# Optimization experiments

Hardware: AMD Instinct MI355X
Metric: run time of the kernel (lower is better)

Reference implementation:

```python
import jax, jax.numpy as jnp
import numpy as np

B, N, DIM, HEADS, RED = 8, 1024, 768, 12, 2
CR = DIM // RED  # 384 reduced channel dim
HD = CR // HEADS  # 32 head dim
EPS = 1e-5


def layer_norm(x, g, b):
    mu = jnp.mean(x, axis=-1, keepdims=True)
    var = jnp.var(x, axis=-1, keepdims=True)
    return (x - mu) * jax.lax.rsqrt(var + EPS) * g + b


def setup_inputs() -> dict:
    key = jax.random.key(0)
    ks = jax.random.split(key, 8)
    s_in = 1.0 / np.sqrt(DIM)
    s_cr = 1.0 / np.sqrt(CR)
    return {
        "x": jax.random.normal(ks[0], (B, N, DIM), dtype=jnp.float32),
        "ln0_g": jnp.ones((DIM,), jnp.float32),
        "ln0_b": jnp.zeros((DIM,), jnp.float32),
        "w_proj": jax.random.normal(ks[1], (CR, DIM), jnp.float32) * s_in,  # conv1x1 -> linear
        "b_proj": jnp.zeros((CR,), jnp.float32),
        "ln1_g": jnp.ones((CR,), jnp.float32),
        "ln1_b": jnp.zeros((CR,), jnp.float32),
        "wq": jax.random.normal(ks[2], (CR, CR), jnp.float32) * s_cr,
        "wk": jax.random.normal(ks[3], (CR, CR), jnp.float32) * s_cr,
        "wv": jax.random.normal(ks[4], (CR, CR), jnp.float32) * s_cr,
    }


def attention(y, wq, wk, wv):
    # y: [B, N, CR]; 1x1 conv == linear on channel dim
    def heads(w):
        return (y @ w.T).reshape(B, N, HEADS, HD).transpose(0, 2, 1, 3)  # [B,H,N,D]
    q, k, v = heads(wq), heads(wk), heads(wv)
    scale = HD ** -0.5
    attn = jax.nn.softmax(jnp.einsum("bhnd,bhmd->bhnm", q, k) * scale, axis=-1)
    out = jnp.einsum("bhnm,bhmd->bhnd", attn, v)  # [B,H,N,D]
    return out.transpose(0, 2, 1, 3).reshape(B, N, CR)


def reference(x, ln0_g, ln0_b, w_proj, b_proj, ln1_g, ln1_b, wq, wk, wv):
    h = layer_norm(x, ln0_g, ln0_b) @ w_proj.T + b_proj  # [B,N,CR]
    y = layer_norm(h, ln1_g, ln1_b)
    return h + attention(y, wq, wk, wv)
```

## Files before the change

### kernel.cpp

```cpp
#include <hip/hip_runtime.h>
#include <math.h>

#define BB 8
#define NN 1024
#define DIM 768
#define HEADS 12
#define CR 384
#define HD 32
#define MROWS (BB*NN)
#define EPS 1e-5f
#define SCALE_Q 0.25503486f

typedef __attribute__((ext_vector_type(8))) __bf16 bf16x8;
typedef __attribute__((ext_vector_type(8))) unsigned short u16x8;
typedef __attribute__((ext_vector_type(4))) float f32x4;

__device__ __forceinline__ unsigned short f2bf(float f) {
    unsigned int u = __float_as_uint(f);
    u += 0x7fffu + ((u >> 16) & 1u);
    return (unsigned short)(u >> 16);
}

__device__ __forceinline__ unsigned int packbf2(float lo, float hi) {
    return (unsigned int)f2bf(lo) | ((unsigned int)f2bf(hi) << 16);
}

__device__ __forceinline__ void async_cp16(const unsigned short* g, unsigned short* l) {
    __builtin_amdgcn_global_load_lds(
        (const __attribute__((address_space(1))) unsigned int*)g,
        (__attribute__((address_space(3))) unsigned int*)l, 16, 0, 0);
}

__global__ __launch_bounds__(256) void ln_bf16(
    const float* __restrict__ A, int K,
    const float* __restrict__ g, const float* __restrict__ bt,
    unsigned short* __restrict__ Y)
{
    const int row = blockIdx.x;
    const int t = threadIdx.x;
    const int nv = K >> 2;
    const float* a = A + (size_t)row * K;
    float4 val = make_float4(0.f, 0.f, 0.f, 0.f);
    float s = 0.f, ss = 0.f;
    if (t < nv) {
        val = ((const float4*)a)[t];
        s = val.x + val.y + val.z + val.w;
        ss = val.x * val.x + val.y * val.y + val.z * val.z + val.w * val.w;
    }
    for (int off = 32; off; off >>= 1) {
        s  += __shfl_down(s, off, 64);
        ss += __shfl_down(ss, off, 64);
    }
    __shared__ float rS[4], rSS[4];
    __shared__ float sh_mu, sh_rs;
    int lane = t & 63, w = t >> 6;
    if (lane == 0) { rS[w] = s; rSS[w] = ss; }
    __syncthreads();
    if (t == 0) {
        float S = rS[0] + rS[1] + rS[2] + rS[3];
        float SS = rSS[0] + rSS[1] + rSS[2] + rSS[3];
        float m = S / K;
        sh_mu = m;
        sh_rs = rsqrtf(SS / K - m * m + EPS);
    }
    __syncthreads();
    if (t < nv) {
        float m = sh_mu, r = sh_rs;
        float4 gv = ((const float4*)g)[t];
        float4 bv = ((const float4*)bt)[t];
        ushort4 o = make_ushort4(
            f2bf((val.x - m) * r * gv.x + bv.x),
            f2bf((val.y - m) * r * gv.y + bv.y),
            f2bf((val.z - m) * r * gv.z + bv.z),
            f2bf((val.w - m) * r * gv.w + bv.w));
        ((ushort4*)(Y + (size_t)row * K))[t] = o;
    }
}

__global__ __launch_bounds__(256) void cast_weights(
    const float* __restrict__ wp, const float* __restrict__ wq,
    const float* __restrict__ wk, const float* __restrict__ wv,
    unsigned short* __restrict__ wpo, unsigned short* __restrict__ wqkvo)
{
    int i = blockIdx.x * 256 + threadIdx.x;
    const float* src; unsigned short* dst; int off;
    if (i < 73728) { src = wp; dst = wpo; off = i; }
    else {
        int j = i - 73728;
        int sel = j / 36864; off = j % 36864;
        src = sel == 0 ? wq : (sel == 1 ? wk : wv);
        dst = wqkvo + (size_t)sel * 147456;
    }
    float4 v = ((const float4*)src)[off];
    ushort4 o = make_ushort4(f2bf(v.x), f2bf(v.y), f2bf(v.z), f2bf(v.w));
    ((ushort4*)dst)[off] = o;
}

template<int KD, int MODE>
__global__ __launch_bounds__(256) void gemm_mfma(
    const unsigned short* __restrict__ A,
    const unsigned short* __restrict__ W,
    const float* __restrict__ bias,
    void* __restrict__ C0, void* __restrict__ C1)
{
    __shared__ unsigned short Asm[2 * 128 * 32];
    __shared__ unsigned short Bsm[2 * 128 * 32];
    const int t = threadIdx.x;
    const int wave = t >> 6, lane = t & 63;
    const int l15 = lane & 15, quad = lane >> 4;
    const int m0 = blockIdx.y * 128;
    const int n0 = blockIdx.x * 128;
    const int wm = (wave & 1) * 64, wn = (wave >> 1) * 64;

    const int srow = lane >> 2;
    const int skq  = (lane & 3) * 8;
    const unsigned short* gA = A + (size_t)(m0 + wave * 32 + srow) * KD + skq;
    const unsigned short* gB = W + (size_t)(n0 + wave * 32 + srow) * KD + skq;
    unsigned short* lA = Asm + wave * 1024;
    unsigned short* lB = Bsm + wave * 1024;

    constexpr int NIT = KD / 32;
    async_cp16(gA, lA);
    async_cp16(gA + (size_t)16 * KD, lA + 512);
    async_cp16(gB, lB);
    async_cp16(gB + (size_t)16 * KD, lB + 512);

    f32x4 acc[4][4];
#pragma unroll
    for (int i = 0; i < 4; i++)
#pragma unroll
        for (int j = 0; j < 4; j++) acc[i][j] = (f32x4){0.f, 0.f, 0.f, 0.f};

    for (int it = 0; it < NIT; it++) {
        __syncthreads();
        const int cur = it & 1;
        if (it + 1 < NIT) {
            const int noff = (cur ^ 1) * 4096;
            async_cp16(gA + (it + 1) * 32, lA + noff);
            async_cp16(gA + (size_t)16 * KD + (it + 1) * 32, lA + noff + 512);
            async_cp16(gB + (it + 1) * 32, lB + noff);
            async_cp16(gB + (size_t)16 * KD + (it + 1) * 32, lB + noff + 512);
        }
        const unsigned short* Ab = Asm + cur * 4096;
        const unsigned short* Bb = Bsm + cur * 4096;
        bf16x8 af[4], bfr[4];
#pragma unroll
        for (int i = 0; i < 4; i++)
            af[i] = *(const bf16x8*)(Ab + (wm + i * 16 + l15) * 32 + quad * 8);
#pragma unroll
        for (int j = 0; j < 4; j++)
            bfr[j] = *(const bf16x8*)(Bb + (wn + j * 16 + l15) * 32 + quad * 8);
#pragma unroll
        for (int i = 0; i < 4; i++)
#pragma unroll
            for (int j = 0; j < 4; j++)
                acc[i][j] = __builtin_amdgcn_mfma_f32_16x16x32_bf16(af[i], bfr[j], acc[i][j], 0, 0, 0);
    }

    if constexpr (MODE == 0) {
        float* C = (float*)C0;
        float bv[4];
#pragma unroll
        for (int j = 0; j < 4; j++) bv[j] = bias[n0 + wn + j * 16 + l15];
#pragma unroll
        for (int i = 0; i < 4; i++)
#pragma unroll
            for (int j = 0; j < 4; j++)
#pragma unroll
                for (int reg = 0; reg < 4; reg++) {
                    int row = m0 + wm + i * 16 + quad * 4 + reg;
                    int col = n0 + wn + j * 16 + l15;
                    C[(size_t)row * CR + col] = acc[i][j][reg] + bv[j];
                }
    } else {
        unsigned short* Cqk = (unsigned short*)C0;
        unsigned short* Vt  = (unsigned short*)C1;
#pragma unroll
        for (int i = 0; i < 4; i++)
#pragma unroll
            for (int j = 0; j < 4; j++) {
                const int colbase = n0 + wn + j * 16;
                const int token0 = m0 + wm + i * 16 + quad * 4;
                if (colbase < DIM) {
                    const float sc = (colbase < CR) ? SCALE_Q : 1.f;
#pragma unroll
                    for (int reg = 0; reg < 4; reg++)
                        Cqk[(size_t)(token0 + reg) * DIM + colbase + l15] = f2bf(acc[i][j][reg] * sc);
                } else {
                    const int ch = colbase - DIM + l15;
                    uint2 pk;
                    pk.x = packbf2(acc[i][j][0], acc[i][j][1]);
                    pk.y = packbf2(acc[i][j][2], acc[i][j][3]);
                    *(uint2*)(Vt + (size_t)ch * MROWS + token0) = pk;
                }
            }
    }
}

__global__ __launch_bounds__(256) void attn_mfma(
    const unsigned short* __restrict__ qk,
    const unsigned short* __restrict__ vt,
    const float* __restrict__ h, float* __restrict__ out)
{
    const int qt = blockIdx.x;
    const int bh = blockIdx.y;
    const int b = bh / HEADS, head = bh % HEADS;
    const int hc = head * HD;
    const int t = threadIdx.x;
    const int wave = t >> 6, lane = t & 63;
    const int l15 = lane & 15, quad = lane >> 4;
    const int q0 = qt * 64;

    __shared__ unsigned short Ks[64 * 40];
    __shared__ unsigned short Vs[32 * 72];
    __shared__ unsigned short Ps[4][16 * 72];
    unsigned short* Pw = Ps[wave];

    bf16x8 qa = *(const bf16x8*)(qk + (size_t)(b * NN + q0 + wave * 16 + l15) * DIM + hc + quad * 8);

    const int rr = t >> 2, seg = t & 3;
    const unsigned short* gK = qk + (size_t)(b * NN + rr) * DIM + CR + hc + seg * 8;
    const int vch = wave * 8 + (lane >> 3), vko = (lane & 7) * 8;
    const unsigned short* gV = vt + (size_t)(hc + vch) * MROWS + b * NN + vko;

    u16x8 kreg = *(const u16x8*)gK;
    u16x8 vreg = *(const u16x8*)gV;

    f32x4 o[2] = {{0.f,0.f,0.f,0.f},{0.f,0.f,0.f,0.f}};
    float lpart = 0.f;

    for (int kt = 0; kt < 16; kt++) {
        __syncthreads();
        *(u16x8*)(Ks + rr * 40 + seg * 8) = kreg;
        *(u16x8*)(Vs + vch * 72 + vko) = vreg;
        if (kt < 15) {
            kreg = *(const u16x8*)(gK + (size_t)(kt + 1) * 64 * DIM);
            vreg = *(const u16x8*)(gV + (kt + 1) * 64);
        }
        __syncthreads();

        f32x4 s[4];
#pragma unroll
        for (int nt = 0; nt < 4; nt++) {
            bf16x8 kb = *(const bf16x8*)(Ks + (nt * 16 + l15) * 40 + quad * 8);
            f32x4 z = {0.f, 0.f, 0.f, 0.f};
            s[nt] = __builtin_amdgcn_mfma_f32_16x16x32_bf16(kb, qa, z, 0, 0, 0);
        }

#pragma unroll
        for (int nt = 0; nt < 4; nt++) {
            float e0 = __builtin_amdgcn_exp2f(s[nt][0]);
            float e1 = __builtin_amdgcn_exp2f(s[nt][1]);
            float e2 = __builtin_amdgcn_exp2f(s[nt][2]);
            float e3 = __builtin_amdgcn_exp2f(s[nt][3]);
            lpart += (e0 + e1) + (e2 + e3);
            uint2 pk;
            pk.x = packbf2(e0, e1);
            pk.y = packbf2(e2, e3);
            *(uint2*)(Pw + l15 * 72 + nt * 16 + quad * 4) = pk;
        }

#pragma unroll
        for (int kk = 0; kk < 2; kk++) {
            bf16x8 pa = *(const bf16x8*)(Pw + l15 * 72 + kk * 32 + quad * 8);
#pragma unroll
            for (int nt2 = 0; nt2 < 2; nt2++) {
                bf16x8 vb = *(const bf16x8*)(Vs + (nt2 * 16 + l15) * 72 + kk * 32 + quad * 8);
                o[nt2] = __builtin_amdgcn_mfma_f32_16x16x32_bf16(pa, vb, o[nt2], 0, 0, 0);
            }
        }
    }

    lpart += __shfl_xor(lpart, 16, 64);
    lpart += __shfl_xor(lpart, 32, 64);
    const float linv = 1.f / lpart;

#pragma unroll
    for (int reg = 0; reg < 4; reg++) {
        const float li = __shfl(linv, quad * 4 + reg, 64);
        const size_t row = (size_t)(b * NN + q0 + wave * 16 + quad * 4 + reg);
#pragma unroll
        for (int nt2 = 0; nt2 < 2; nt2++) {
            size_t idx = row * CR + hc + nt2 * 16 + l15;
            out[idx] = h[idx] + o[nt2][reg] * li;
        }
    }
}

extern "C" void kernel_launch(void* const* d_in, const int* in_sizes, int n_in,
                              void* d_out, int out_size, void* d_ws, size_t ws_size,
                              hipStream_t stream) {
    const float* x      = (const float*)d_in[0];
    const float* ln0_g  = (const float*)d_in[1];
    const float* ln0_b  = (const float*)d_in[2];
    const float* w_proj = (const float*)d_in[3];
    const float* b_proj = (const float*)d_in[4];
    const float* ln1_g  = (const float*)d_in[5];
    const float* ln1_b  = (const float*)d_in[6];
    const float* wq     = (const float*)d_in[7];
    const float* wk     = (const float*)d_in[8];
    const float* wv     = (const float*)d_in[9];
    float* out = (float*)d_out;

    char* base = (char*)d_ws;
    unsigned short* a0   = (unsigned short*)base;
    unsigned short* qkb  = (unsigned short*)base;
    float*          hbuf = (float*)(base + 12582912);
    unsigned short* yb   = (unsigned short*)(base + 25165824);
    unsigned short* vtb  = (unsigned short*)(base + 31457280);
    unsigned short* wp   = (unsigned short*)(base + 37748736);
    unsigned short* wqkv = (unsigned short*)(base + 38338560);

    ln_bf16<<<MROWS, 256, 0, stream>>>(x, DIM, ln0_g, ln0_b, a0);
    cast_weights<<<720, 256, 0, stream>>>(w_proj, wq, wk, wv, wp, wqkv);
    gemm_mfma<DIM, 0><<<dim3(CR / 128, MROWS / 128), 256, 0, stream>>>(
        a0, wp, b_proj, hbuf, nullptr);
    ln_bf16<<<MROWS, 256, 0, stream>>>(hbuf, CR, ln1_g, ln1_b, yb);
    gemm_mfma<CR, 1><<<dim3(1152 / 128, MROWS / 128), 256, 0, stream>>>(
        yb, wqkv, nullptr, qkb, vtb);
    attn_mfma<<<dim3(NN / 64, BB * HEADS), 256, 0, stream>>>(qkb, vtb, hbuf, out);
}
```

Before: 176.1 us.

## Split-K projection GEMM, fuse weight cast into LN0, widen attention query tile

Merges the weight cast into the first layernorm launch, saving one kernel launch. Splits the K=768 projection GEMM into two halves along a grid z dimension so the 192-block grid gets twice as many blocks. The partial sums and the bias are then added inside a new ln1 kernel, which also writes h. Each attention wave now handles 32 query rows and reuses the K and V fragments it loads, halving the grid, at the cost of more registers. The extra partial-sum buffer adds global memory traffic and needs a larger workspace.

```diff
diff --git a/kernel.cpp b/kernel.cpp
--- a/kernel.cpp
+++ b/kernel.cpp
@@ -31,15 +31,32 @@
         (__attribute__((address_space(3))) unsigned int*)l, 16, 0, 0);
 }
 
-__global__ __launch_bounds__(256) void ln_bf16(
-    const float* __restrict__ A, int K,
+__global__ __launch_bounds__(256) void ln0_cast(
+    const float* __restrict__ x,
     const float* __restrict__ g, const float* __restrict__ bt,
-    unsigned short* __restrict__ Y)
+    unsigned short* __restrict__ a0,
+    const float* __restrict__ wp, const float* __restrict__ wq,
+    const float* __restrict__ wk, const float* __restrict__ wv,
+    unsigned short* __restrict__ wpo, unsigned short* __restrict__ wqkvo)
 {
-    const int row = blockIdx.x;
+    const int bx = blockIdx.x;
     const int t = threadIdx.x;
-    const int nv = K >> 2;
-    const float* a = A + (size_t)row * K;
+    if (bx >= MROWS) {
+        int i = (bx - MROWS) * 256 + t;
+        const float* src; unsigned short* dst; int off;
+        if (i < 73728) { src = wp; dst = wpo; off = i; }
+        else {
+            int j = i - 73728;
+            int sel = j / 36864; off = j % 36864;
+            src = sel == 0 ? wq : (sel == 1 ? wk : wv);
+            dst = wqkvo + (size_t)sel * 147456;
+        }
+        float4 v = ((const float4*)src)[off];
+        ((ushort4*)dst)[off] = make_ushort4(f2bf(v.x), f2bf(v.y), f2bf(v.z), f2bf(v.w));
+        return;
+    }
+    const int nv = DIM >> 2;
+    const float* a = x + (size_t)bx * DIM;
     float4 val = make_float4(0.f, 0.f, 0.f, 0.f);
     float s = 0.f, ss = 0.f;
     if (t < nv) {
@@ -59,48 +76,77 @@
     if (t == 0) {
         float S = rS[0] + rS[1] + rS[2] + rS[3];
         float SS = rSS[0] + rSS[1] + rSS[2] + rSS[3];
-        float m = S / K;
+        float m = S / DIM;
         sh_mu = m;
-        sh_rs = rsqrtf(SS / K - m * m + EPS);
+        sh_rs = rsqrtf(SS / DIM - m * m + EPS);
     }
     __syncthreads();
     if (t < nv) {
         float m = sh_mu, r = sh_rs;
         float4 gv = ((const float4*)g)[t];
         float4 bv = ((const float4*)bt)[t];
-        ushort4 o = make_ushort4(
+        ((ushort4*)(a0 + (size_t)bx * DIM))[t] = make_ushort4(
             f2bf((val.x - m) * r * gv.x + bv.x),
             f2bf((val.y - m) * r * gv.y + bv.y),
             f2bf((val.z - m) * r * gv.z + bv.z),
             f2bf((val.w - m) * r * gv.w + bv.w));
-        ((ushort4*)(Y + (size_t)row * K))[t] = o;
-    }
-}
-
-__global__ __launch_bounds__(256) void cast_weights(
-    const float* __restrict__ wp, const float* __restrict__ wq,
-    const float* __restrict__ wk, const float* __restrict__ wv,
-    unsigned short* __restrict__ wpo, unsigned short* __restrict__ wqkvo)
+    }
+}
+
+__global__ __launch_bounds__(128) void ln1_sum(
+    const float* __restrict__ h0, const float* __restrict__ h1,
+    const float* __restrict__ bias,
+    const float* __restrict__ g, const float* __restrict__ bt,
+    float* __restrict__ hs, unsigned short* __restrict__ y)
 {
-    int i = blockIdx.x * 256 + threadIdx.x;
-    const float* src; unsigned short* dst; int off;
-    if (i < 73728) { src = wp; dst = wpo; off = i; }
-    else {
-        int j = i - 73728;
-        int sel = j / 36864; off = j % 36864;
-        src = sel == 0 ? wq : (sel == 1 ? wk : wv);
-        dst = wqkvo + (size_t)sel * 147456;
-    }
-    float4 v = ((const float4*)src)[off];
-    ushort4 o = make_ushort4(f2bf(v.x), f2bf(v.y), f2bf(v.z), f2bf(v.w));
-    ((ushort4*)dst)[off] = o;
-}
-
-template<int KD, int MODE>
+    const int row = blockIdx.x;
+    const int t = threadIdx.x;
+    const int nv = CR >> 2;
+    float4 val = make_float4(0.f, 0.f, 0.f, 0.f);
+    float s = 0.f, ss = 0.f;
+    if (t < nv) {
+        float4 v0 = ((const float4*)(h0 + (size_t)row * CR))[t];
+        float4 v1 = ((const float4*)(h1 + (size_t)row * CR))[t];
+        float4 bv = ((const float4*)bias)[t];
+        val = make_float4(v0.x + v1.x + bv.x, v0.y + v1.y + bv.y,
+                          v0.z + v1.z + bv.z, v0.w + v1.w + bv.w);
+        ((float4*)(hs + (size_t)row * CR))[t] = val;
+        s = val.x + val.y + val.z + val.w;
+        ss = val.x * val.x + val.y * val.y + val.z * val.z + val.w * val.w;
+    }
+    for (int off = 32; off; off >>= 1) {
+        s  += __shfl_down(s, off, 64);
+        ss += __shfl_down(ss, off, 64);
+    }
+    __shared__ float rS[2], rSS[2];
+    __shared__ float sh_mu, sh_rs;
+    int lane = t & 63, w = t >> 6;
+    if (lane == 0) { rS[w] = s; rSS[w] = ss; }
+    __syncthreads();
+    if (t == 0) {
+        float S = rS[0] + rS[1];
+        float SS = rSS[0] + rSS[1];
+        float m = S / CR;
+        sh_mu = m;
+        sh_rs = rsqrtf(SS / CR - m * m + EPS);
+    }
+    __syncthreads();
+    if (t < nv) {
+        float m = sh_mu, r = sh_rs;
+        float4 gv = ((const float4*)g)[t];
+        float4 bv = ((const float4*)bt)[t];
+        ((ushort4*)(y + (size_t)row * CR))[t] = make_ushort4(
+            f2bf((val.x - m) * r * gv.x + bv.x),
+            f2bf((val.y - m) * r * gv.y + bv.y),
+            f2bf((val.z - m) * r * gv.z + bv.z),
+            f2bf((val.w - m) * r * gv.w + bv.w));
+    }
+}
+
+template<int KD, int NITER, int MODE>
 __global__ __launch_bounds__(256) void gemm_mfma(
     const unsigned short* __restrict__ A,
     const unsigned short* __restrict__ W,
-    const float* __restrict__ bias,
     void* __restrict__ C0, void* __restrict__ C1)
 {
     __shared__ unsigned short Asm[2 * 128 * 32];
@@ -110,16 +156,16 @@
     const int l15 = lane & 15, quad = lane >> 4;
     const int m0 = blockIdx.y * 128;
     const int n0 = blockIdx.x * 128;
+    const int koff = blockIdx.z * (NITER * 32);
     const int wm = (wave & 1) * 64, wn = (wave >> 1) * 64;
 
     const int srow = lane >> 2;
     const int skq  = (lane & 3) * 8;
-    const unsigned short* gA = A + (size_t)(m0 + wave * 32 + srow) * KD + skq;
-    const unsigned short* gB = W + (size_t)(n0 + wave * 32 + srow) * KD + skq;
+    const unsigned short* gA = A + (size_t)(m0 + wave * 32 + srow) * KD + koff + skq;
+    const unsigned short* gB = W + (size_t)(n0 + wave * 32 + srow) * KD + koff + skq;
     unsigned short* lA = Asm + wave * 1024;
     unsigned short* lB = Bsm + wave * 1024;
 
-    constexpr int NIT = KD / 32;
     async_cp16(gA, lA);
     async_cp16(gA + (size_t)16 * KD, lA + 512);
     async_cp16(gB, lB);
@@ -131,10 +177,10 @@
 #pragma unroll
         for (int j = 0; j < 4; j++) acc[i][j] = (f32x4){0.f, 0.f, 0.f, 0.f};
 
-    for (int it = 0; it < NIT; it++) {
+    for (int it = 0; it < NITER; it++) {
         __syncthreads();
         const int cur = it & 1;
-        if (it + 1 < NIT) {
+        if (it + 1 < NITER) {
             const int noff = (cur ^ 1) * 4096;
             async_cp16(gA + (it + 1) * 32, lA + noff);
             async_cp16(gA + (size_t)16 * KD + (it + 1) * 32, lA + noff + 512);
@@ -158,10 +204,7 @@
     }
 
     if constexpr (MODE == 0) {
-        float* C = (float*)C0;
-        float bv[4];
-#pragma unroll
-        for (int j = 0; j < 4; j++) bv[j] = bias[n0 + wn + j * 16 + l15];
+        float* C = (float*)C0 + (size_t)blockIdx.z * MROWS * CR;
 #pragma unroll
         for (int i = 0; i < 4; i++)
 #pragma unroll
@@ -170,7 +213,7 @@
                 for (int reg = 0; reg < 4; reg++) {
                     int row = m0 + wm + i * 16 + quad * 4 + reg;
                     int col = n0 + wn + j * 16 + l15;
-                    C[(size_t)row * CR + col] = acc[i][j][reg] + bv[j];
+                    C[(size_t)row * CR + col] = acc[i][j][reg];
                 }
     } else {
         unsigned short* Cqk = (unsigned short*)C0;
@@ -209,14 +252,18 @@
     const int t = threadIdx.x;
     const int wave = t >> 6, lane = t & 63;
     const int l15 = lane & 15, quad = lane >> 4;
-    const int q0 = qt * 64;
+    const int q0 = qt * 128;
 
     __shared__ unsigned short Ks[64 * 40];
     __shared__ unsigned short Vs[32 * 72];
-    __shared__ unsigned short Ps[4][16 * 72];
+    __shared__ unsigned short Ps[4][32 * 72];
     unsigned short* Pw = Ps[wave];
 
-    bf16x8 qa = *(const bf16x8*)(qk + (size_t)(b * NN + q0 + wave * 16 + l15) * DIM + hc + quad * 8);
+    bf16x8 qa[2];
+#pragma unroll
+    for (int qi = 0; qi < 2; qi++)
+        qa[qi] = *(const bf16x8*)(qk + (size_t)(b * NN + q0 + wave * 32 + qi * 16 + l15) * DIM
+                                  + hc + quad * 8);
 
     const int rr = t >> 2, seg = t & 3;
     const unsigned short* gK = qk + (size_t)(b * NN + rr) * DIM + CR + hc + seg * 8;
@@ -226,8 +273,9 @@
     u16x8 kreg = *(const u16x8*)gK;
     u16x8 vreg = *(const u16x8*)gV;
 
-    f32x4 o[2] = {{0.f,0.f,0.f,0.f},{0.f,0.f,0.f,0.f}};
-    float lpart = 0.f;
+    f32x4 o[2][2] = {{{0.f,0.f,0.f,0.f},{0.f,0.f,0.f,0.f}},
+                     {{0.f,0.f,0.f,0.f},{0.f,0.f,0.f,0.f}}};
+    float lpart[2] = {0.f, 0.f};
 
     for (int kt = 0; kt < 16; kt++) {
         __syncthreads();
@@ -239,50 +287,66 @@
         }
         __syncthreads();
 
-        f32x4 s[4];
-#pragma unroll
-        for (int nt = 0; nt < 4; nt++) {
-            bf16x8 kb = *(const bf16x8*)(Ks + (nt * 16 + l15) * 40 + quad * 8);
-            f32x4 z = {0.f, 0.f, 0.f, 0.f};
-            s[nt] = __builtin_amdgcn_mfma_f32_16x16x32_bf16(kb, qa, z, 0, 0, 0);
-        }
-
-#pragma unroll
-        for (int nt = 0; nt < 4; nt++) {
-            float e0 = __builtin_amdgcn_exp2f(s[nt][0]);
-            float e1 = __builtin_amdgcn_exp2f(s[nt][1]);
-            float e2 = __builtin_amdgcn_exp2f(s[nt][2]);
-            float e3 = __builtin_amdgcn_exp2f(s[nt][3]);
-            lpart += (e0 + e1) + (e2 + e3);
-            uint2 pk;
-            pk.x = packbf2(e0, e1);
-            pk.y = packbf2(e2, e3);
-            *(uint2*)(Pw + l15 * 72 + nt * 16 + quad * 4) = pk;
-        }
-
-#pragma unroll
-        for (int kk = 0; kk < 2; kk++) {
-            bf16x8 pa = *(const bf16x8*)(Pw + l15 * 72 + kk * 32 + quad * 8);
+        bf16x8 kb[4];
+#pragma unroll
+        for (int nt = 0; nt < 4; nt++)
+            kb[nt] = *(const bf16x8*)(Ks + (nt * 16 + l15) * 40 + quad * 8);
+
+#pragma unroll
+        for (int qi = 0; qi < 2; qi++) {
+            f32x4 s[4];
+#pragma unroll
+            for (int nt = 0; nt < 4; nt++) {
+                f32x4 z = {0.f, 0.f, 0.f, 0.f};
+                s[nt] = __builtin_amdgcn_mfma_f32_16x16x32_bf16(kb[nt], qa[qi], z, 0, 0, 0);
+            }
+#pragma unroll
+            for (int nt = 0; nt < 4; nt++) {
+                float e0 = __builtin_amdgcn_exp2f(s[nt][0]);
+                float e1 = __builtin_amdgcn_exp2f(s[nt][1]);
+                float e2 = __builtin_amdgcn_exp2f(s[nt][2]);
+                float e3 = __builtin_amdgcn_exp2f(s[nt][3]);
+                lpart[qi] += (e0 + e1) + (e2 + e3);
+                uint2 pk;
+                pk.x = packbf2(e0, e1);
+                pk.y = packbf2(e2, e3);
+                *(uint2*)(Pw + (qi * 16 + l15) * 72 + nt * 16 + quad * 4) = pk;
+            }
+        }
+
+        bf16x8 vb[2][2];
+#pragma unroll
+        for (int kk = 0; kk < 2; kk++)
+#pragma unroll
+            for (int nt2 = 0; nt2 < 2; nt2++)
+                vb[kk][nt2] = *(const bf16x8*)(Vs + (nt2 * 16 + l15) * 72 + kk * 32 + quad * 8);
+
+#pragma unroll
+        for (int qi = 0; qi < 2; qi++)
+#pragma unroll
+            for (int kk = 0; kk < 2; kk++) {
+                bf16x8 pa = *(const bf16x8*)(Pw + (qi * 16 + l15) * 72 + kk * 32 + quad * 8);
+#pragma unroll
+                for (int nt2 = 0; nt2 < 2; nt2++)
+                    o[qi][nt2] = __builtin_amdgcn_mfma_f32_16x16x32_bf16(pa, vb[kk][nt2], o[qi][nt2], 0, 0, 0);
+            }
+    }
+
+#pragma unroll
+    for (int qi = 0; qi < 2; qi++) {
+        float l = lpart[qi];
+        l += __shfl_xor(l, 16, 64);
+        l += __shfl_xor(l, 32, 64);
+        const float linv = 1.f / l;
+#pragma unroll
+        for (int reg = 0; reg < 4; reg++) {
+            const float li = __shfl(linv, quad * 4 + reg, 64);
+            const size_t row = (size_t)(b * NN + q0 + wave * 32 + qi * 16 + quad * 4 + reg);
 #pragma unroll
             for (int nt2 = 0; nt2 < 2; nt2++) {
-                bf16x8 vb = *(const bf16x8*)(Vs + (nt2 * 16 + l15) * 72 + kk * 32 + quad * 8);
-                o[nt2] = __builtin_amdgcn_mfma_f32_16x16x32_bf16(pa, vb, o[nt2], 0, 0, 0);
-            }
-        }
-    }
-
-    lpart += __shfl_xor(lpart, 16, 64);
-    lpart += __shfl_xor(lpart, 32, 64);
-    const float linv = 1.f / lpart;
-
-#pragma unroll
-    for (int reg = 0; reg < 4; reg++) {
-        const float li = __shfl(linv, quad * 4 + reg, 64);
-        const size_t row = (size_t)(b * NN + q0 + wave * 16 + quad * 4 + reg);
-#pragma unroll
-        for (int nt2 = 0; nt2 < 2; nt2++) {
-            size_t idx = row * CR + hc + nt2 * 16 + l15;
-            out[idx] = h[idx] + o[nt2][reg] * li;
+                size_t idx = row * CR + hc + nt2 * 16 + l15;
+                out[idx] = h[idx] + o[qi][nt2][reg] * li;
+            }
         }
     }
 }
@@ -305,18 +369,20 @@
     char* base = (char*)d_ws;
     unsigned short* a0   = (unsigned short*)base;
     unsigned short* qkb  = (unsigned short*)base;
-    float*          hbuf = (float*)(base + 12582912);
-    unsigned short* yb   = (unsigned short*)(base + 25165824);
-    unsigned short* vtb  = (unsigned short*)(base + 31457280);
-    unsigned short* wp   = (unsigned short*)(base + 37748736);
-    unsigned short* wqkv = (unsigned short*)(base + 38338560);
-
-    ln_bf16<<<MROWS, 256, 0, stream>>>(x, DIM, ln0_g, ln0_b, a0);
-    cast_weights<<<720, 256, 0, stream>>>(w_proj, wq, wk, wv, wp, wqkv);
-    gemm_mfma<DIM, 0><<<dim3(CR / 128, MROWS / 128), 256, 0, stream>>>(
-        a0, wp, b_proj, hbuf, nullptr);
-    ln_bf16<<<MROWS, 256, 0, stream>>>(hbuf, CR, ln1_g, ln1_b, yb);
-    gemm_mfma<CR, 1><<<dim3(1152 / 128, MROWS / 128), 256, 0, stream>>>(
-        yb, wqkv, nullptr, qkb, vtb);
-    attn_mfma<<<dim3(NN / 64, BB * HEADS), 256, 0, stream>>>(qkb, vtb, hbuf, out);
-}
+    float*          hp   = (float*)(base + 12582912);
+    float*          hbuf = (float*)(base + 37748736);
+    unsigned short* yb   = (unsigned short*)(base + 50331648);
+    unsigned short* vtb  = (unsigned short*)(base + 56623104);
+    unsigned short* wp   = (unsigned short*)(base + 62914560);
+    unsigned short* wqkv = (unsigned short*)(base + 63504384);
+
+    ln0_cast<<<MROWS + 720, 256, 0, stream>>>(x, ln0_g, ln0_b, a0,
+                                              w_proj, wq, wk, wv, wp, wqkv);
+    gemm_mfma<DIM, 12, 0><<<dim3(CR / 128, MROWS / 128, 2), 256, 0, stream>>>(
+        a0, wp, hp, nullptr);
+    ln1_sum<<<MROWS, 128, 0, stream>>>(hp, hp + (size_t)MROWS * CR, b_proj,
+                                       ln1_g, ln1_b, hbuf, yb);
+    gemm_mfma<CR, 12, 1><<<dim3(1152 / 128, MROWS / 128, 1), 256, 0, stream>>>(
+        yb, wqkv, qkb, vtb);
+    attn_mfma<<<dim3(NN / 128, BB * HEADS), 256, 0, stream>>>(qkb, vtb, hbuf, out);
+}
```

After: 165.3 us. -6.1%, faster.
